# Performance work log

Hardware: AMD Instinct MI355X
Metric: run time of the kernel (lower is better)

Reference implementation:

```python
import jax, jax.numpy as jnp
import numpy as np

VOCAB=20000; EMB=300; FEAT=2052; HID=1024; OUT=3000; NK=8; NS=10; KOBJ=36; B=256; QLEN=14

def _wn(key, shape, scale=0.05):
    return jax.random.normal(key, shape, dtype=jnp.float32)*scale

def setup_inputs() -> dict:
    key = jax.random.key(0)
    ks = jax.random.split(key, 40)
    inp = {}
    inp['question'] = jax.random.randint(ks[0], (B, QLEN), 0, VOCAB)
    inp['image'] = jax.random.uniform(ks[1], (B, KOBJ, FEAT), dtype=jnp.float32)
    inp['K'] = KOBJ
    inp['qlen'] = jax.random.randint(ks[2], (B,), 1, QLEN+1)
    # params
    inp['wembed'] = _wn(ks[3], (VOCAB, EMB), 0.1)
    # GRU params (torch layout: W_ih [3H,E], W_hh [3H,H], biases [3H]) order r,z,n
    inp['gru_wih'] = _wn(ks[4], (3*HID, EMB))
    inp['gru_whh'] = _wn(ks[5], (3*HID, HID))
    inp['gru_bih'] = jnp.zeros((3*HID,), jnp.float32)
    inp['gru_bhh'] = jnp.zeros((3*HID,), jnp.float32)
    # img_attention (VisualAttention on feat_dim -> hid)
    inp['ia_img_w'] = _wn(ks[6], (HID, FEAT)); inp['ia_img_b'] = jnp.zeros((HID,), jnp.float32)
    inp['ia_txt_w'] = _wn(ks[7], (HID, HID)); inp['ia_txt_b'] = jnp.zeros((HID,), jnp.float32)
    inp['ia_att_w'] = _wn(ks[8], (1, HID)); inp['ia_att_b'] = jnp.zeros((1,), jnp.float32)
    # graph_attention (on feat_dim+hid -> hid)
    inp['ga_img_w'] = _wn(ks[9], (HID, FEAT+HID)); inp['ga_img_b'] = jnp.zeros((HID,), jnp.float32)
    inp['ga_txt_w'] = _wn(ks[10], (HID, HID)); inp['ga_txt_b'] = jnp.zeros((HID,), jnp.float32)
    inp['ga_att_w'] = _wn(ks[11], (1, HID)); inp['ga_att_b'] = jnp.zeros((1,), jnp.float32)
    # graph conv 1: feat_dim -> 2*hid, NK kernels, coord_dim=2
    inp['gc1_mu'] = _wn(ks[12], (NK, 2), 0.5)
    inp['gc1_sigma'] = jnp.ones((NK, 2), jnp.float32)*0.5
    inp['gc1_w'] = _wn(ks[13], (NK, FEAT, (2*HID)//NK), 0.02)
    inp['gc1_b'] = jnp.zeros((2*HID,), jnp.float32)
    # graph conv 2: 2*hid -> hid
    inp['gc2_mu'] = _wn(ks[14], (NK, 2), 0.5)
    inp['gc2_sigma'] = jnp.ones((NK, 2), jnp.float32)*0.5
    inp['gc2_w'] = _wn(ks[15], (NK, 2*HID, HID//NK), 0.02)
    inp['gc2_b'] = jnp.zeros((HID,), jnp.float32)
    # output heads
    inp['out1_w'] = _wn(ks[16], (OUT, HID)); inp['out1_b'] = jnp.zeros((OUT,), jnp.float32)
    inp['out2_w'] = _wn(ks[17], (OUT, OUT)); inp['out2_b'] = jnp.zeros((OUT,), jnp.float32)
    inp['iout1_w'] = _wn(ks[18], (OUT, HID)); inp['iout1_b'] = jnp.zeros((OUT,), jnp.float32)
    inp['iout2_w'] = _wn(ks[19], (OUT, OUT)); inp['iout2_b'] = jnp.zeros((OUT,), jnp.float32)
    return inp

def _gru_encode(question, qlen, wembed, wih, whh, bih, bhh):
    emb = wembed[question]  # [B,T,E]
    T = emb.shape[1]
    def step(h, xt_t):
        xt, t = xt_t
        gi = xt @ wih.T + bih
        gh = h @ whh.T + bhh
        ir, iz, inn = jnp.split(gi, 3, axis=-1)
        hr, hz, hn = jnp.split(gh, 3, axis=-1)
        r = jax.nn.sigmoid(ir + hr)
        z = jax.nn.sigmoid(iz + hz)
        n = jnp.tanh(inn + r*hn)
        hnew = (1-z)*n + z*h
        valid = (t < qlen)[:, None]
        h = jnp.where(valid, hnew, h)
        return h, None
    h0 = jnp.zeros((emb.shape[0], HID), emb.dtype)
    hT, _ = jax.lax.scan(step, h0, (jnp.swapaxes(emb,0,1), jnp.arange(T)))
    return hT

def _vis_att(img, q, img_w, img_b, txt_w, txt_b, att_w, att_b):
    img_proj = jax.nn.relu(img @ img_w.T + img_b)        # [B,L,H]
    q_proj = jax.nn.relu(q @ txt_w.T + txt_b)            # [B,H]
    joint = img_proj * q_proj[:, None, :]
    raw = joint @ att_w.T + att_b                         # [B,L,1]
    att = jax.nn.softmax(raw, axis=1)[..., 0]             # [B,L]
    img_att = jnp.einsum('bli,bl->bi', img, att)
    comb = jax.nn.relu(img_att @ img_w.T + img_b) * q_proj
    return att, comb

def _gauss_weights(pseudo, mu, sigma):
    # pseudo [B,N,N,2], mu/sigma [NK,2] -> [B,N,N,NK]
    diff = pseudo[..., None, :] - mu  # [B,N,N,NK,2]
    w = jnp.exp(-0.5 * jnp.sum((diff / (1e-14 + sigma))**2, axis=-1))
    return w

def _graph_conv(neigh, pseudo, mu, sigma, w, b):
    # neigh [B,N,N,Fin], pseudo [B,N,N,2], w [NK,Fin,Fout//NK]
    kw = _gauss_weights(pseudo, mu, sigma)                # [B,N,N,K]
    agg = jnp.einsum('bnmf,bnmk->bnkf', neigh, kw)        # weighted sum over neighbours
    out = jnp.einsum('bnkf,kfo->bnko', agg, w)            # per-kernel linear
    B_, N_, K_, O_ = out.shape
    return out.reshape(B_, N_, K_*O_) + b

def _compute_pseudo(bb_centre):
    d = bb_centre[:, :, None, :] - bb_centre[:, None, :, :]  # [B,N,N,2]
    rho = jnp.sqrt(d[..., 0]**2 + d[..., 1]**2)
    theta = jnp.arctan2(d[..., 0], d[..., 1])
    return jnp.stack((rho, theta), axis=-1)

def reference(question, image, K, qlen, wembed, gru_wih, gru_whh, gru_bih, gru_bhh,
              ia_img_w, ia_img_b, ia_txt_w, ia_txt_b, ia_att_w, ia_att_b,
              ga_img_w, ga_img_b, ga_txt_w, ga_txt_b, ga_att_w, ga_att_b,
              gc1_mu, gc1_sigma, gc1_w, gc1_b, gc2_mu, gc2_sigma, gc2_w, gc2_b,
              out1_w, out1_b, out2_w, out2_b, iout1_w, iout1_b, iout2_w, iout2_b):
    qenc = _gru_encode(question, qlen, wembed, gru_wih, gru_whh, gru_bih, gru_bhh)  # [B,H]
    att, img_ques_comb = _vis_att(image, qenc, ia_img_w, ia_img_b, ia_txt_w, ia_txt_b, ia_att_w, ia_att_b)
    _, topk_idx = jax.lax.top_k(att, NS)                  # [B,NS]
    topk_img = jnp.take_along_axis(image, topk_idx[:, :, None], axis=1)  # [B,NS,F]
    bb = topk_img[:, :, -4:]
    bb_size = bb[:, :, 2:] - bb[:, :, :2]
    bb_centre = bb[:, :, :2] + 0.5*bb_size
    pseudo = _compute_pseudo(bb_centre)                    # [B,NS,NS,2]
    neigh1 = jnp.broadcast_to(topk_img[:, None, :, :], (topk_img.shape[0], NS, NS, topk_img.shape[-1]))
    h1 = jax.nn.relu(_graph_conv(neigh1, pseudo, gc1_mu, gc1_sigma, gc1_w, gc1_b))  # [B,NS,2H]
    neigh2 = jnp.broadcast_to(h1[:, None, :, :], (h1.shape[0], NS, NS, h1.shape[-1]))
    h2 = jax.nn.relu(_graph_conv(neigh2, pseudo, gc2_mu, gc2_sigma, gc2_w, gc2_b))  # [B,NS,H]
    graph_nodes = jnp.concatenate((topk_img, h2), axis=2)  # [B,NS,F+H]
    g_att, graph_ques_comb = _vis_att(graph_nodes, qenc, ga_img_w, ga_img_b, ga_txt_w, ga_txt_b, ga_att_w, ga_att_b)
    logits_1 = jax.nn.relu(graph_ques_comb @ out1_w.T + out1_b) @ out2_w.T + out2_b
    logits_2 = jax.nn.relu(img_ques_comb @ iout1_w.T + iout1_b) @ iout2_w.T + iout2_b
    return logits_1 + logits_2
```

## Files before the change

kernel.cpp:

```cpp
#include <hip/hip_runtime.h>
#include <cmath>

#define VOCAB 20000
#define EMB 300
#define FEAT 2052
#define HID 1024
#define OUTN 3000
#define NK 8
#define NS 10
#define KOBJ 36
#define BATCH 256
#define QLEN_ 14

typedef __attribute__((ext_vector_type(8))) short bf8v;
typedef __attribute__((ext_vector_type(4))) float f4v;

__device__ __forceinline__ short f2bf(float f) {
    union { float f; unsigned u; } v; v.f = f;
    unsigned r = v.u + 0x7fff + ((v.u >> 16) & 1);
    return (short)(r >> 16);
}
__device__ __forceinline__ float bf2f(short h) {
    union { unsigned u; float f; } v; v.u = ((unsigned)(unsigned short)h) << 16;
    return v.f;
}

__device__ __forceinline__ void gload16(const short* g, short* l) {
    typedef __attribute__((address_space(1))) void gv;
    typedef __attribute__((address_space(3))) void lv;
    __builtin_amdgcn_global_load_lds((gv*)g, (lv*)l, 16, 0, 0);
}

template<int N> __device__ __forceinline__ void vmw() {
    asm volatile("s_waitcnt vmcnt(%0)" :: "n"(N) : "memory");
}
template<int PW> __device__ __forceinline__ void vmwait(int nf) {
    switch (nf) {
        case 0:  vmw<0>();      break;
        case 1:  vmw<1 * PW>(); break;
        case 2:  vmw<2 * PW>(); break;
        default: vmw<3 * PW>(); break;
    }
}

template<int PREC, int MI, int D>
__global__ __launch_bounds__(512)
void mgemm_k(const short* __restrict__ Ah_g, const short* __restrict__ Al_g, int lda,
             const short* __restrict__ Bh_g, const short* __restrict__ Bl_g, int ldb,
             float* __restrict__ Cf, int ldc,
             short* __restrict__ Cb, int ldcb,
             const float* __restrict__ bias,
             const float* __restrict__ mul, int ldmul,
             int Nvalid, int K, int beta, int relu)
{
    constexpr int BM  = MI * 32;
    constexpr int MIW = MI / 2;
    constexpr int ASZ = BM * 32;
    constexpr int BSZ = 128 * 32;
    constexpr int NBUF = (PREC == 3) ? 2 * D : D;
    __shared__ short SA[NBUF * ASZ];
    __shared__ short SB[NBUF * BSZ];

    int gx = gridDim.x;
    int flat = blockIdx.y * gx + blockIdx.x;
    int total = gx * gridDim.y;
    int bx, by;
    if ((total & 7) == 0) {
        int r = (flat & 7) * (total >> 3) + (flat >> 3);
        by = r / gx; bx = r - by * gx;
    } else { bx = blockIdx.x; by = blockIdx.y; }

    int tid = threadIdx.x;
    int lane = tid & 63, wid = tid >> 6;
    int m0 = by * BM, n0 = bx * 128;
    const short* Ab  = Ah_g + (size_t)m0 * lda;
    const short* Bb  = Bh_g + (size_t)n0 * ldb;
    const short* Abl = (PREC == 3) ? Al_g + (size_t)m0 * lda : nullptr;
    const short* Bbl = (PREC == 3) ? Bl_g + (size_t)n0 * ldb : nullptr;

    constexpr int AISS = BM / 16;
    constexpr int NISS = (PREC == 3) ? 2 * (AISS + 8) : (AISS + 8);
    constexpr int REM  = NISS & 7;
    constexpr int PWH  = (NISS + 7) >> 3;
    constexpr int PWL  = NISS >> 3;
    int rr = lane & 15;
    int cc = (lane >> 4) * 8;

    auto stage = [&](int q, int k0) {
        short* sa  = SA + q * ASZ;
        short* sb  = SB + q * BSZ;
        short* sal = SA + (D + q) * ASZ;
        short* sbl = SB + (D + q) * BSZ;
        #pragma unroll
        for (int t = wid; t < NISS; t += 8) {
            int u = t;
            const short* g; short* l;
            if (u < AISS)              {                   g = Ab  + (size_t)(u*16+rr)*lda + k0 + cc; l = sa  + u*512; }
            else if (u < AISS + 8)     { u -= AISS;        g = Bb  + (size_t)(u*16+rr)*ldb + k0 + cc; l = sb  + u*512; }
            else if (u < 2*AISS + 8)   { u -= AISS + 8;    g = Abl + (size_t)(u*16+rr)*lda + k0 + cc; l = sal + u*512; }
            else                       { u -= 2*AISS + 8;  g = Bbl + (size_t)(u*16+rr)*ldb + k0 + cc; l = sbl + u*512; }
            gload16(g, l);
        }
    };

    f4v acc[MIW][4] = {};
    int nk = K >> 5;
    int P = (D - 1 < nk) ? (D - 1) : nk;
    for (int q = 0; q < P; ++q) stage(q, q << 5);

    for (int kt = 0; kt < nk; ++kt) {
        int nxt = kt + D - 1;
        if (nxt < nk) stage(nxt & (D - 1), nxt << 5);
        int rem = nk - 1 - kt;
        int nf = rem < D - 1 ? rem : D - 1;
        if (REM == 0 || wid < REM) vmwait<PWH>(nf); else vmwait<PWL>(nf);
        __builtin_amdgcn_s_barrier();
        __builtin_amdgcn_sched_barrier(0);
        {
            int q = kt & (D - 1);
            int wy = wid >> 1, wx = wid & 1;
            int quad = lane >> 4, l15 = lane & 15;
            const bf8v* A8 = (const bf8v*)(SA + q * ASZ);
            const bf8v* B8 = (const bf8v*)(SB + q * BSZ);
            bf8v ah[MIW], bh[4];
            #pragma unroll
            for (int i = 0; i < MIW; i++) ah[i] = A8[(wy*MIW + i)*64 + quad*16 + l15];
            #pragma unroll
            for (int j = 0; j < 4; j++)   bh[j] = B8[(wx*4 + j)*64 + quad*16 + l15];
            if (PREC == 3) {
                const bf8v* A8l = (const bf8v*)(SA + (D + q) * ASZ);
                const bf8v* B8l = (const bf8v*)(SB + (D + q) * BSZ);
                bf8v al[MIW], bl[4];
                #pragma unroll
                for (int i = 0; i < MIW; i++) al[i] = A8l[(wy*MIW + i)*64 + quad*16 + l15];
                #pragma unroll
                for (int j = 0; j < 4; j++)   bl[j] = B8l[(wx*4 + j)*64 + quad*16 + l15];
                #pragma unroll
                for (int i = 0; i < MIW; i++)
                    #pragma unroll
                    for (int j = 0; j < 4; j++) {
                        acc[i][j] = __builtin_amdgcn_mfma_f32_16x16x32_bf16(ah[i], bh[j], acc[i][j], 0, 0, 0);
                        acc[i][j] = __builtin_amdgcn_mfma_f32_16x16x32_bf16(al[i], bh[j], acc[i][j], 0, 0, 0);
                        acc[i][j] = __builtin_amdgcn_mfma_f32_16x16x32_bf16(ah[i], bl[j], acc[i][j], 0, 0, 0);
                    }
            } else {
                #pragma unroll
                for (int i = 0; i < MIW; i++)
                    #pragma unroll
                    for (int j = 0; j < 4; j++)
                        acc[i][j] = __builtin_amdgcn_mfma_f32_16x16x32_bf16(ah[i], bh[j], acc[i][j], 0, 0, 0);
            }
        }
        __builtin_amdgcn_sched_barrier(0);
        __builtin_amdgcn_s_barrier();
        __builtin_amdgcn_sched_barrier(0);
    }

    int wy = wid >> 1, wx = wid & 1;
    int quad = lane >> 4, l15 = lane & 15;
    #pragma unroll
    for (int i = 0; i < MIW; i++) {
        int mb = m0 + wy * (MIW * 16) + i * 16 + quad * 4;
        #pragma unroll
        for (int j = 0; j < 4; j++) {
            int n = n0 + wx * 64 + j * 16 + l15;
            bool nin = n < Nvalid;
            #pragma unroll
            for (int r = 0; r < 4; r++) {
                int m = mb + r;
                float v = acc[i][j][r];
                if (nin) {
                    if (beta) v += Cf[(size_t)m * ldc + n];
                    if (bias) v += bias[n];
                    if (relu) v = fmaxf(v, 0.f);
                    if (mul)  v *= mul[(size_t)m * ldmul + n];
                    if (Cf) Cf[(size_t)m * ldc + n] = v;
                    if (Cb) Cb[(size_t)m * ldcb + n] = f2bf(v);
                } else if (Cb && n < ldcb) {
                    Cb[(size_t)m * ldcb + n] = 0;
                }
            }
        }
    }
}

static void mg(hipStream_t s, int prec, int mi,
               const short* Ah, const short* Al, int lda,
               const short* Bh, const short* Bl, int ldb,
               float* Cf, int ldc, short* Cb, int ldcb,
               const float* bias, const float* mul, int ldmul,
               int M, int N, int K, int beta, int relu)
{
    dim3 grid((N + 127) / 128, M / (mi * 32));
    if (prec == 3) {
        if (mi == 4) mgemm_k<3,4,2><<<grid,512,0,s>>>(Ah,Al,lda,Bh,Bl,ldb,Cf,ldc,Cb,ldcb,bias,mul,ldmul,N,K,beta,relu);
        else         mgemm_k<3,2,2><<<grid,512,0,s>>>(Ah,Al,lda,Bh,Bl,ldb,Cf,ldc,Cb,ldcb,bias,mul,ldmul,N,K,beta,relu);
    } else {
        if (mi == 4) mgemm_k<1,4,4><<<grid,512,0,s>>>(Ah,Al,lda,Bh,Bl,ldb,Cf,ldc,Cb,ldcb,bias,mul,ldmul,N,K,beta,relu);
        else         mgemm_k<1,2,4><<<grid,512,0,s>>>(Ah,Al,lda,Bh,Bl,ldb,Cf,ldc,Cb,ldcb,bias,mul,ldmul,N,K,beta,relu);
    }
}

__global__ void fill0_k(float* p, int n) {
    int i = blockIdx.x * 256 + threadIdx.x;
    if (i < n) p[i] = 0.f;
}

__global__ void cvt_k(const float* __restrict__ src, int sld, int srows, int scols,
                      short* __restrict__ hi, short* __restrict__ lo, int dld, int n) {
    int i = blockIdx.x * 256 + threadIdx.x;
    if (i >= n) return;
    int r = i / dld, c = i - r * dld;
    float v = (r < srows && c < scols) ? src[(size_t)r * sld + c] : 0.f;
    short h = f2bf(v);
    hi[i] = h;
    if (lo) lo[i] = f2bf(v - bf2f(h));
}

__global__ void embed_k(const int* __restrict__ q, const float* __restrict__ wemb,
                        short* __restrict__ hi, short* __restrict__ lo) {
    int i = blockIdx.x * 256 + threadIdx.x;
    if (i >= BATCH * QLEN_ * 320) return;
    int c = i % 320; int bt = i / 320;
    float v = (c < EMB) ? wemb[(size_t)q[bt] * EMB + c] : 0.f;
    short h = f2bf(v);
    hi[i] = h;
    lo[i] = f2bf(v - bf2f(h));
}

__global__ void gru_point_k(const float* __restrict__ gi, int ldgi, const float* __restrict__ gh,
                            const int* __restrict__ qlen, float* __restrict__ h,
                            short* __restrict__ qh, short* __restrict__ ql, int t) {
    int i = blockIdx.x * 256 + threadIdx.x;
    if (i >= BATCH * HID) return;
    int b = i / HID; int j = i % HID;
    float ir = gi[(size_t)b * ldgi + j];
    float iz = gi[(size_t)b * ldgi + HID + j];
    float in = gi[(size_t)b * ldgi + 2 * HID + j];
    float hr = gh[(size_t)b * 3 * HID + j];
    float hz = gh[(size_t)b * 3 * HID + HID + j];
    float hn = gh[(size_t)b * 3 * HID + 2 * HID + j];
    float r = 1.f / (1.f + expf(-(ir + hr)));
    float z = 1.f / (1.f + expf(-(iz + hz)));
    float n = tanhf(in + r * hn);
    float hold = h[i];
    float val = (t < qlen[b]) ? ((1.f - z) * n + z * hold) : hold;
    h[i] = val;
    short hh = f2bf(val);
    qh[i] = hh;
    ql[i] = f2bf(val - bf2f(hh));
}

__global__ __launch_bounds__(256)
void attraw_k(const float* __restrict__ proj, const float* __restrict__ qproj,
              const float* __restrict__ attw, const float* __restrict__ attb,
              float* __restrict__ raw, int L) {
    int wave = blockIdx.x * 4 + (threadIdx.x >> 6);
    int lane = threadIdx.x & 63;
    if (wave >= BATCH * L) return;
    int b = wave / L;
    const float* p = proj + (size_t)wave * HID;
    const float* q = qproj + (size_t)b * HID;
    float s = 0.f;
    for (int hh = lane; hh < HID; hh += 64) s += p[hh] * q[hh] * attw[hh];
    #pragma unroll
    for (int o = 32; o; o >>= 1) s += __shfl_down(s, o, 64);
    if (lane == 0) raw[wave] = s + attb[0];
}

__global__ void softmax_k(float* raw, int L) {
    int b = blockIdx.x * blockDim.x + threadIdx.x;
    if (b >= BATCH) return;
    float* r = raw + (size_t)b * L;
    float mx = -1e30f;
    for (int l = 0; l < L; l++) mx = fmaxf(mx, r[l]);
    float sum = 0.f;
    for (int l = 0; l < L; l++) { float e = expf(r[l] - mx); r[l] = e; sum += e; }
    float inv = 1.f / sum;
    for (int l = 0; l < L; l++) r[l] *= inv;
}

__global__ void wsumb_k(const float* __restrict__ src, int sF, const float* __restrict__ att,
                        int L, short* __restrict__ outh, int dld, int n) {
    int i = blockIdx.x * 256 + threadIdx.x;
    if (i >= n) return;
    int c = i % dld; int b = i / dld;
    float s = 0.f;
    if (c < sF)
        for (int l = 0; l < L; l++) s += src[((size_t)b * L + l) * sF + c] * att[b * L + l];
    outh[i] = f2bf(s);
}

__global__ void topk_k(const float* __restrict__ att, int* __restrict__ idx) {
    int b = blockIdx.x * blockDim.x + threadIdx.x;
    if (b >= BATCH) return;
    float v[KOBJ]; bool taken[KOBJ];
    for (int l = 0; l < KOBJ; l++) { v[l] = att[(size_t)b * KOBJ + l]; taken[l] = false; }
    for (int s = 0; s < NS; s++) {
        float best = -1e30f; int bi = 0;
        for (int l = 0; l < KOBJ; l++)
            if (!taken[l] && v[l] > best) { best = v[l]; bi = l; }
        taken[bi] = true;
        idx[b * NS + s] = bi;
    }
}

__global__ void gather_k(const float* __restrict__ img, const int* __restrict__ idx,
                         float* __restrict__ outf, short* __restrict__ outh) {
    int i = blockIdx.x * 256 + threadIdx.x;
    if (i >= BATCH * NS * 2080) return;
    int c = i % 2080; int bs = i / 2080; int b = bs / NS; int s = bs % NS;
    float v = 0.f;
    if (c < FEAT) {
        v = img[((size_t)b * KOBJ + idx[b * NS + s]) * FEAT + c];
        outf[(size_t)bs * FEAT + c] = v;
    }
    outh[i] = f2bf(v);
}

__global__ void kw_k(const float* __restrict__ image, const int* __restrict__ tidx,
                     const float* __restrict__ mu1, const float* __restrict__ sig1,
                     const float* __restrict__ mu2, const float* __restrict__ sig2,
                     float* __restrict__ kw1, float* __restrict__ kw2) {
    int i = blockIdx.x * blockDim.x + threadIdx.x;
    if (i >= BATCH * NS * NS) return;
    int m = i % NS; int bn = i / NS; int b = bn / NS; int n = bn % NS;
    const float* bbn = image + ((size_t)b * KOBJ + tidx[b * NS + n]) * FEAT + (FEAT - 4);
    const float* bbm = image + ((size_t)b * KOBJ + tidx[b * NS + m]) * FEAT + (FEAT - 4);
    float cnx = bbn[0] + 0.5f * (bbn[2] - bbn[0]);
    float cny = bbn[1] + 0.5f * (bbn[3] - bbn[1]);
    float cmx = bbm[0] + 0.5f * (bbm[2] - bbm[0]);
    float cmy = bbm[1] + 0.5f * (bbm[3] - bbm[1]);
    float d0 = cnx - cmx, d1 = cny - cmy;
    float rho = sqrtf(d0 * d0 + d1 * d1);
    float theta = atan2f(d0, d1);
    #pragma unroll
    for (int k = 0; k < NK; k++) {
        float a1 = (rho   - mu1[k * 2 + 0]) / (1e-14f + sig1[k * 2 + 0]);
        float b1 = (theta - mu1[k * 2 + 1]) / (1e-14f + sig1[k * 2 + 1]);
        kw1[(size_t)i * NK + k] = expf(-0.5f * (a1 * a1 + b1 * b1));
        float a2 = (rho   - mu2[k * 2 + 0]) / (1e-14f + sig2[k * 2 + 0]);
        float b2 = (theta - mu2[k * 2 + 1]) / (1e-14f + sig2[k * 2 + 1]);
        kw2[(size_t)i * NK + k] = expf(-0.5f * (a2 * a2 + b2 * b2));
    }
}

__global__ void mix_k(const float* __restrict__ Y, const float* __restrict__ kw,
                      const float* __restrict__ bias, short* __restrict__ outh,
                      float* __restrict__ outf, int KO, int CT) {
    int i = blockIdx.x * blockDim.x + threadIdx.x;
    if (i >= BATCH * NS * CT) return;
    int c = i % CT; int bn = i / CT; int b = bn / NS;
    int k = c / KO;
    float s = bias[c];
    const float* kwp = kw + ((size_t)bn * NS) * NK + k;
    const float* Yp  = Y + ((size_t)b * NS) * CT + c;
    #pragma unroll
    for (int m = 0; m < NS; m++) s += kwp[m * NK] * Yp[(size_t)m * CT];
    s = fmaxf(s, 0.f);
    outh[i] = f2bf(s);
    if (outf) outf[i] = s;
}

__global__ void packcvt_k(const float* __restrict__ src, short* __restrict__ dst,
                          int S, int O, int dld) {
    __shared__ float t[32][33];
    int k = blockIdx.z;
    const float* s = src + (size_t)k * S * O;
    short* d = dst + (size_t)k * O * dld;
    int f0 = blockIdx.y * 32, o0 = blockIdx.x * 32;
    for (int i = threadIdx.y; i < 32; i += 8) {
        int f = f0 + i, o = o0 + threadIdx.x;
        t[i][threadIdx.x] = (f < S && o < O) ? s[(size_t)f * O + o] : 0.f;
    }
    __syncthreads();
    for (int i = threadIdx.y; i < 32; i += 8) {
        int o = o0 + i, f = f0 + threadIdx.x;
        if (o < O && f < dld) d[(size_t)o * dld + f] = f2bf(t[threadIdx.x][i]);
    }
}

extern "C" void kernel_launch(void* const* d_in, const int* in_sizes, int n_in,
                              void* d_out, int out_size, void* d_ws, size_t ws_size,
                              hipStream_t stream)
{
    const int*   question  = (const int*)d_in[0];
    const float* image     = (const float*)d_in[1];
    const int*   qlen      = (const int*)d_in[3];
    const float* wembed    = (const float*)d_in[4];
    const float* gru_wih   = (const float*)d_in[5];
    const float* gru_whh   = (const float*)d_in[6];
    const float* gru_bih   = (const float*)d_in[7];
    const float* gru_bhh   = (const float*)d_in[8];
    const float* ia_img_w  = (const float*)d_in[9];
    const float* ia_img_b  = (const float*)d_in[10];
    const float* ia_txt_w  = (const float*)d_in[11];
    const float* ia_txt_b  = (const float*)d_in[12];
    const float* ia_att_w  = (const float*)d_in[13];
    const float* ia_att_b  = (const float*)d_in[14];
    const float* ga_img_w  = (const float*)d_in[15];
    const float* ga_img_b  = (const float*)d_in[16];
    const float* ga_txt_w  = (const float*)d_in[17];
    const float* ga_txt_b  = (const float*)d_in[18];
    const float* ga_att_w  = (const float*)d_in[19];
    const float* ga_att_b  = (const float*)d_in[20];
    const float* gc1_mu    = (const float*)d_in[21];
    const float* gc1_sigma = (const float*)d_in[22];
    const float* gc1_w     = (const float*)d_in[23];
    const float* gc1_b     = (const float*)d_in[24];
    const float* gc2_mu    = (const float*)d_in[25];
    const float* gc2_sigma = (const float*)d_in[26];
    const float* gc2_w     = (const float*)d_in[27];
    const float* gc2_b     = (const float*)d_in[28];
    const float* out1_w    = (const float*)d_in[29];
    const float* out1_b    = (const float*)d_in[30];
    const float* out2_w    = (const float*)d_in[31];
    const float* out2_b    = (const float*)d_in[32];
    const float* iout1_w   = (const float*)d_in[33];
    const float* iout1_b   = (const float*)d_in[34];
    const float* iout2_w   = (const float*)d_in[35];
    const float* iout2_b   = (const float*)d_in[36];
    float* out = (float*)d_out;

    float* ws = (float*)d_ws;
    size_t off = 0;
    auto alloc  = [&](size_t n)   { size_t o = off; off += (n + 63) & ~(size_t)63; return ws + o; };
    auto allocS = [&](size_t nsh) { return (short*)alloc((nsh + 1) >> 1); };

    float* qenc   = alloc((size_t)BATCH * HID);
    float* att_ia = alloc((size_t)BATCH * KOBJ);
    float* att_ga = alloc((size_t)BATCH * NS);
    int*   tidx   = (int*)alloc((size_t)BATCH * NS);
    float* timg_f = alloc((size_t)2560 * FEAT);
    float* kw1    = alloc((size_t)BATCH * NS * NS * NK);
    float* kw2    = alloc((size_t)BATCH * NS * NS * NK);
    short* wih_h   = allocS((size_t)3072 * 320);  short* wih_l   = allocS((size_t)3072 * 320);
    short* whh_h   = allocS((size_t)3072 * 1024); short* whh_l   = allocS((size_t)3072 * 1024);
    short* iaimg_h = allocS((size_t)1024 * 2080); short* iaimg_l = allocS((size_t)1024 * 2080);
    short* iatxt_h = allocS((size_t)1024 * 1024); short* iatxt_l = allocS((size_t)1024 * 1024);
    short* emb_h   = allocS((size_t)3584 * 320);  short* emb_l   = allocS((size_t)3584 * 320);
    short* qenc_h  = allocS((size_t)256 * 1024);  short* qenc_l  = allocS((size_t)256 * 1024);
    float* R1 = alloc(12500000);
    float* U  = alloc(19200000);

    float* gi_all = R1;
    float* gh     = R1 + 11010048;
    float* improj = R1;
    float* qproj  = R1 + 9437184;
    short* img_h  = (short*)U;
    short* img_l  = (short*)U + 19169280;
    short* imatt_h = (short*)U + 13189120;
    float* Y1 = R1;
    float* Y2 = R1 + 5242880;
    short* gc1t_h = (short*)(R1 + 7864320);
    short* gc2t_h = (short*)(R1 + 7864320) + 4259840;
    short* timg_h = (short*)U;
    short* h1_h   = (short*)U + 5324800;
    short* h2_h   = (short*)U + 10567680;
    float* h2_f   = (float*)((short*)U + 20807680);
    float* gproj   = R1;
    float* qproj2  = R1 + 2621440;
    float* gtmp    = R1 + 2883584;
    short* gatt_img_h = (short*)U + 13721600;
    short* gatt_h2_h  = (short*)U + 14254080;
    short* gcomb_h = (short*)U + 14516224;
    short* icomb_h = (short*)U + 14778368;
    short* hid1_h  = (short*)U + 15040512;
    short* hid2_h  = (short*)U + 15810560;
    short* gaw_img_h = (short*)U + 16580608;
    short* gaw_h2_h  = (short*)U + 18710528;
    short* gatxt_h   = (short*)U + 19759104;
    short* o1w_h  = (short*)R1;
    short* io1w_h = (short*)R1 + 3145728;
    short* o2w_h  = (short*)R1 + 6291456;
    short* io2w_h = (short*)R1 + 15532032;

    auto NB = [](size_t n) { return (unsigned)((n + 255) / 256); };

    cvt_k<<<NB(983040),  256, 0, stream>>>(gru_wih, 300, 3072, 300, wih_h, wih_l, 320, 983040);
    cvt_k<<<NB(3145728), 256, 0, stream>>>(gru_whh, 1024, 3072, 1024, whh_h, whh_l, 1024, 3145728);
    cvt_k<<<NB(2129920), 256, 0, stream>>>(ia_img_w, FEAT, 1024, FEAT, iaimg_h, iaimg_l, 2080, 2129920);
    cvt_k<<<NB(1048576), 256, 0, stream>>>(ia_txt_w, 1024, 1024, 1024, iatxt_h, iatxt_l, 1024, 1048576);
    cvt_k<<<NB(19169280),256, 0, stream>>>(image, FEAT, 9216, FEAT, img_h, img_l, 2080, 19169280);
    embed_k<<<NB(1146880), 256, 0, stream>>>(question, wembed, emb_h, emb_l);
    fill0_k<<<NB(262144), 256, 0, stream>>>(qenc, 262144);
    fill0_k<<<NB(262144), 256, 0, stream>>>((float*)qenc_h, 262144);

    mg(stream, 3, 4, emb_h, emb_l, 320, wih_h, wih_l, 320, gi_all, 3072, nullptr, 0,
       gru_bih, nullptr, 0, 3584, 3072, 320, 0, 0);
    for (int t = 0; t < QLEN_; t++) {
        mg(stream, 3, 2, qenc_h, qenc_l, 1024, whh_h, whh_l, 1024, gh, 3072, nullptr, 0,
           gru_bhh, nullptr, 0, 256, 3072, 1024, 0, 0);
        gru_point_k<<<NB(262144), 256, 0, stream>>>(gi_all + (size_t)t * 3 * HID, QLEN_ * 3 * HID,
                                                    gh, qlen, qenc, qenc_h, qenc_l, t);
    }

    mg(stream, 3, 4, img_h, img_l, 2080, iaimg_h, iaimg_l, 2080, improj, 1024, nullptr, 0,
       ia_img_b, nullptr, 0, 9216, 1024, 2080, 0, 1);
    mg(stream, 3, 2, qenc_h, qenc_l, 1024, iatxt_h, iatxt_l, 1024, qproj, 1024, nullptr, 0,
       ia_txt_b, nullptr, 0, 256, 1024, 1024, 0, 1);
    attraw_k<<<(BATCH * KOBJ) / 4, 256, 0, stream>>>(improj, qproj, ia_att_w, ia_att_b, att_ia, KOBJ);
    softmax_k<<<1, 256, 0, stream>>>(att_ia, KOBJ);
    wsumb_k<<<NB(532480), 256, 0, stream>>>(image, FEAT, att_ia, KOBJ, imatt_h, 2080, 532480);
    mg(stream, 1, 2, imatt_h, nullptr, 2080, iaimg_h, nullptr, 2080, nullptr, 0, icomb_h, 1024,
       ia_img_b, qproj, 1024, 256, 1024, 2080, 0, 1);

    topk_k<<<1, 256, 0, stream>>>(att_ia, tidx);
    gather_k<<<NB(5324800), 256, 0, stream>>>(image, tidx, timg_f, timg_h);
    kw_k<<<NB(25600), 256, 0, stream>>>(image, tidx, gc1_mu, gc1_sigma, gc2_mu, gc2_sigma, kw1, kw2);
    packcvt_k<<<dim3(8, 65, NK), dim3(32, 8), 0, stream>>>(gc1_w, gc1t_h, FEAT, 256, 2080);
    packcvt_k<<<dim3(4, 64, NK), dim3(32, 8), 0, stream>>>(gc2_w, gc2t_h, 2048, 128, 2048);
    mg(stream, 1, 4, timg_h, nullptr, 2080, gc1t_h, nullptr, 2080, Y1, 2048, nullptr, 0,
       nullptr, nullptr, 0, 2560, 2048, 2080, 0, 0);
    mix_k<<<NB(5242880), 256, 0, stream>>>(Y1, kw1, gc1_b, h1_h, nullptr, 256, 2048);
    mg(stream, 1, 4, h1_h, nullptr, 2048, gc2t_h, nullptr, 2048, Y2, 1024, nullptr, 0,
       nullptr, nullptr, 0, 2560, 1024, 2048, 0, 0);
    mix_k<<<NB(2621440), 256, 0, stream>>>(Y2, kw2, gc2_b, h2_h, h2_f, 128, 1024);

    cvt_k<<<NB(2129920), 256, 0, stream>>>(ga_img_w, FEAT + HID, 1024, FEAT, gaw_img_h, nullptr, 2080, 2129920);
    cvt_k<<<NB(1048576), 256, 0, stream>>>(ga_img_w + FEAT, FEAT + HID, 1024, HID, gaw_h2_h, nullptr, 1024, 1048576);
    cvt_k<<<NB(1048576), 256, 0, stream>>>(ga_txt_w, 1024, 1024, 1024, gatxt_h, nullptr, 1024, 1048576);
    mg(stream, 1, 4, timg_h, nullptr, 2080, gaw_img_h, nullptr, 2080, gproj, 1024, nullptr, 0,
       nullptr, nullptr, 0, 2560, 1024, 2080, 0, 0);
    mg(stream, 1, 4, h2_h, nullptr, 1024, gaw_h2_h, nullptr, 1024, gproj, 1024, nullptr, 0,
       ga_img_b, nullptr, 0, 2560, 1024, 1024, 1, 1);
    mg(stream, 1, 2, qenc_h, nullptr, 1024, gatxt_h, nullptr, 1024, qproj2, 1024, nullptr, 0,
       ga_txt_b, nullptr, 0, 256, 1024, 1024, 0, 1);
    attraw_k<<<(BATCH * NS) / 4, 256, 0, stream>>>(gproj, qproj2, ga_att_w, ga_att_b, att_ga, NS);
    softmax_k<<<1, 256, 0, stream>>>(att_ga, NS);
    wsumb_k<<<NB(532480), 256, 0, stream>>>(timg_f, FEAT, att_ga, NS, gatt_img_h, 2080, 532480);
    wsumb_k<<<NB(262144), 256, 0, stream>>>(h2_f, HID, att_ga, NS, gatt_h2_h, 1024, 262144);
    mg(stream, 1, 2, gatt_img_h, nullptr, 2080, gaw_img_h, nullptr, 2080, gtmp, 1024, nullptr, 0,
       nullptr, nullptr, 0, 256, 1024, 2080, 0, 0);
    mg(stream, 1, 2, gatt_h2_h, nullptr, 1024, gaw_h2_h, nullptr, 1024, gtmp, 1024, gcomb_h, 1024,
       ga_img_b, qproj2, 1024, 256, 1024, 1024, 1, 1);

    cvt_k<<<NB(3145728), 256, 0, stream>>>(out1_w, 1024, OUTN, 1024, o1w_h, nullptr, 1024, 3145728);
    cvt_k<<<NB(3145728), 256, 0, stream>>>(iout1_w, 1024, OUTN, 1024, io1w_h, nullptr, 1024, 3145728);
    cvt_k<<<NB(9240576), 256, 0, stream>>>(out2_w, OUTN, OUTN, OUTN, o2w_h, nullptr, 3008, 9240576);
    cvt_k<<<NB(9240576), 256, 0, stream>>>(iout2_w, OUTN, OUTN, OUTN, io2w_h, nullptr, 3008, 9240576);
    mg(stream, 1, 2, gcomb_h, nullptr, 1024, o1w_h, nullptr, 1024, nullptr, 0, hid1_h, 3008,
       out1_b, nullptr, 0, 256, OUTN, 1024, 0, 1);
    mg(stream, 1, 2, icomb_h, nullptr, 1024, io1w_h, nullptr, 1024, nullptr, 0, hid2_h, 3008,
       iout1_b, nullptr, 0, 256, OUTN, 1024, 0, 1);
    mg(stream, 1, 2, hid1_h, nullptr, 3008, o2w_h, nullptr, 3008, out, OUTN, nullptr, 0,
       out2_b, nullptr, 0, 256, OUTN, 3008, 0, 0);
    mg(stream, 1, 2, hid2_h, nullptr, 3008, io2w_h, nullptr, 3008, out, OUTN, nullptr, 0,
       iout2_b, nullptr, 0, 256, OUTN, 3008, 1, 0);
}
```

Baseline: 1.768 ms.

## Batch paired GEMMs into one launch, split-K GRU recurrence, rewrite graph mix kernel

Extends the GEMM kernel so one launch can run two independent problems by duplicating the grid in y. This is used to split the GRU hidden-state GEMM into two K halves that are summed in the pointwise kernel, and to run the two output-head GEMM chains side by side, adding their results at the end. It also adds an XCD-aware block remap, switches the large GEMMs to 256-row tiles (MI=8), and rewrites the graph-conv mix kernel to stage kernel weights in shared memory and reuse each Y load across all NS outputs. The aim is to fill more CUs on small GEMMs, cut launch count, and reduce redundant global reads. The cost is extra temporary buffers, an extra add kernel, and MI=8 tiles that may raise register and LDS pressure.

```diff
diff --git a/kernel.cpp b/kernel.cpp
--- a/kernel.cpp
+++ b/kernel.cpp
@@ -47,11 +47,15 @@
 __global__ __launch_bounds__(512)
 void mgemm_k(const short* __restrict__ Ah_g, const short* __restrict__ Al_g, int lda,
              const short* __restrict__ Bh_g, const short* __restrict__ Bl_g, int ldb,
-             float* __restrict__ Cf, int ldc,
-             short* __restrict__ Cb, int ldcb,
-             const float* __restrict__ bias,
-             const float* __restrict__ mul, int ldmul,
-             int Nvalid, int K, int beta, int relu)
+             float* __restrict__ Cf_g, int ldc,
+             short* __restrict__ Cb_g, int ldcb,
+             const float* __restrict__ bias_g,
+             const float* __restrict__ mul_g, int ldmul,
+             int Nvalid, int K, int beta, int relu,
+             const short* __restrict__ A2h, const short* __restrict__ A2l,
+             const short* __restrict__ B2h, const short* __restrict__ B2l,
+             float* __restrict__ C2f, short* __restrict__ C2b,
+             const float* __restrict__ bias2)
 {
     constexpr int BM  = MI * 32;
     constexpr int MIW = MI / 2;
@@ -61,22 +65,41 @@
     __shared__ short SA[NBUF * ASZ];
     __shared__ short SB[NBUF * BSZ];
 
-    int gx = gridDim.x;
+    int gx = gridDim.x, gy = gridDim.y;
     int flat = blockIdx.y * gx + blockIdx.x;
-    int total = gx * gridDim.y;
+    int total = gx * gy;
     int bx, by;
-    if ((total & 7) == 0) {
+    if ((total & 7) == 0 && (gx & 7) == 0) {
+        int xcd = flat & 7, r = flat >> 3;
+        int cpx = gx >> 3;
+        int col = r / gy;
+        bx = xcd * cpx + col;
+        by = r - col * gy;
+    } else if ((total & 7) == 0) {
         int r = (flat & 7) * (total >> 3) + (flat >> 3);
         by = r / gx; bx = r - by * gx;
     } else { bx = blockIdx.x; by = blockIdx.y; }
 
+    const short *pAh = Ah_g, *pAl = Al_g, *pBh = Bh_g, *pBl = Bl_g;
+    float* pCf = Cf_g; short* pCb = Cb_g;
+    const float* pbias = bias_g; const float* pmul = mul_g;
+    int pbeta = beta;
+    if (A2h) {
+        int yh = gy >> 1;
+        if (by >= yh) {
+            by -= yh;
+            pAh = A2h; pAl = A2l; pBh = B2h; pBl = B2l;
+            pCf = C2f; pCb = C2b; pbias = bias2; pmul = nullptr; pbeta = 0;
+        }
+    }
+
     int tid = threadIdx.x;
     int lane = tid & 63, wid = tid >> 6;
     int m0 = by * BM, n0 = bx * 128;
-    const short* Ab  = Ah_g + (size_t)m0 * lda;
-    const short* Bb  = Bh_g + (size_t)n0 * ldb;
-    const short* Abl = (PREC == 3) ? Al_g + (size_t)m0 * lda : nullptr;
-    const short* Bbl = (PREC == 3) ? Bl_g + (size_t)n0 * ldb : nullptr;
+    const short* Ab  = pAh + (size_t)m0 * lda;
+    const short* Bb  = pBh + (size_t)n0 * ldb;
+    const short* Abl = (PREC == 3) ? pAl + (size_t)m0 * lda : nullptr;
+    const short* Bbl = (PREC == 3) ? pBl + (size_t)n0 * ldb : nullptr;
 
     constexpr int AISS = BM / 16;
     constexpr int NISS = (PREC == 3) ? 2 * (AISS + 8) : (AISS + 8);
@@ -110,14 +133,14 @@
 
     for (int kt = 0; kt < nk; ++kt) {
         int nxt = kt + D - 1;
-        if (nxt < nk) stage(nxt & (D - 1), nxt << 5);
+        if (nxt < nk) stage(nxt % D, nxt << 5);
         int rem = nk - 1 - kt;
         int nf = rem < D - 1 ? rem : D - 1;
         if (REM == 0 || wid < REM) vmwait<PWH>(nf); else vmwait<PWL>(nf);
         __builtin_amdgcn_s_barrier();
         __builtin_amdgcn_sched_barrier(0);
         {
-            int q = kt & (D - 1);
+            int q = kt % D;
             int wy = wid >> 1, wx = wid & 1;
             int quad = lane >> 4, l15 = lane & 15;
             const bf8v* A8 = (const bf8v*)(SA + q * ASZ);
@@ -170,18 +193,43 @@
                 int m = mb + r;
                 float v = acc[i][j][r];
                 if (nin) {
-                    if (beta) v += Cf[(size_t)m * ldc + n];
-                    if (bias) v += bias[n];
-                    if (relu) v = fmaxf(v, 0.f);
-                    if (mul)  v *= mul[(size_t)m * ldmul + n];
-                    if (Cf) Cf[(size_t)m * ldc + n] = v;
-                    if (Cb) Cb[(size_t)m * ldcb + n] = f2bf(v);
-                } else if (Cb && n < ldcb) {
-                    Cb[(size_t)m * ldcb + n] = 0;
+                    if (pbeta) v += pCf[(size_t)m * ldc + n];
+                    if (pbias) v += pbias[n];
+                    if (relu)  v = fmaxf(v, 0.f);
+                    if (pmul)  v *= pmul[(size_t)m * ldmul + n];
+                    if (pCf) pCf[(size_t)m * ldc + n] = v;
+                    if (pCb) pCb[(size_t)m * ldcb + n] = f2bf(v);
+                } else if (pCb && n < ldcb) {
+                    pCb[(size_t)m * ldcb + n] = 0;
                 }
             }
         }
     }
+}
+
+static void mgx(hipStream_t s, int prec, int mi,
+                const short* Ah, const short* Al, int lda,
+                const short* Bh, const short* Bl, int ldb,
+                float* Cf, int ldc, short* Cb, int ldcb,
+                const float* bias, const float* mul, int ldmul,
+                int M, int N, int K, int beta, int relu,
+                int ydup,
+                const short* A2h, const short* A2l,
+                const short* B2h, const short* B2l,
+                float* C2f, short* C2b, const float* bias2)
+{
+    dim3 grid((N + 127) / 128, (M / (mi * 32)) * ydup);
+    #define ARGS Ah,Al,lda,Bh,Bl,ldb,Cf,ldc,Cb,ldcb,bias,mul,ldmul,N,K,beta,relu,A2h,A2l,B2h,B2l,C2f,C2b,bias2
+    if (prec == 3) {
+        if      (mi == 8) mgemm_k<3,8,2><<<grid,512,0,s>>>(ARGS);
+        else if (mi == 4) mgemm_k<3,4,2><<<grid,512,0,s>>>(ARGS);
+        else              mgemm_k<3,2,2><<<grid,512,0,s>>>(ARGS);
+    } else {
+        if      (mi == 8) mgemm_k<1,8,4><<<grid,512,0,s>>>(ARGS);
+        else if (mi == 4) mgemm_k<1,4,4><<<grid,512,0,s>>>(ARGS);
+        else              mgemm_k<1,2,4><<<grid,512,0,s>>>(ARGS);
+    }
+    #undef ARGS
 }
 
 static void mg(hipStream_t s, int prec, int mi,
@@ -191,14 +239,8 @@
                const float* bias, const float* mul, int ldmul,
                int M, int N, int K, int beta, int relu)
 {
-    dim3 grid((N + 127) / 128, M / (mi * 32));
-    if (prec == 3) {
-        if (mi == 4) mgemm_k<3,4,2><<<grid,512,0,s>>>(Ah,Al,lda,Bh,Bl,ldb,Cf,ldc,Cb,ldcb,bias,mul,ldmul,N,K,beta,relu);
-        else         mgemm_k<3,2,2><<<grid,512,0,s>>>(Ah,Al,lda,Bh,Bl,ldb,Cf,ldc,Cb,ldcb,bias,mul,ldmul,N,K,beta,relu);
-    } else {
-        if (mi == 4) mgemm_k<1,4,4><<<grid,512,0,s>>>(Ah,Al,lda,Bh,Bl,ldb,Cf,ldc,Cb,ldcb,bias,mul,ldmul,N,K,beta,relu);
-        else         mgemm_k<1,2,4><<<grid,512,0,s>>>(Ah,Al,lda,Bh,Bl,ldb,Cf,ldc,Cb,ldcb,bias,mul,ldmul,N,K,beta,relu);
-    }
+    mgx(s, prec, mi, Ah, Al, lda, Bh, Bl, ldb, Cf, ldc, Cb, ldcb, bias, mul, ldmul,
+        M, N, K, beta, relu, 1, nullptr, nullptr, nullptr, nullptr, nullptr, nullptr, nullptr);
 }
 
 __global__ void fill0_k(float* p, int n) {
@@ -229,6 +271,7 @@
 }
 
 __global__ void gru_point_k(const float* __restrict__ gi, int ldgi, const float* __restrict__ gh,
+                            const float* __restrict__ gh2,
                             const int* __restrict__ qlen, float* __restrict__ h,
                             short* __restrict__ qh, short* __restrict__ ql, int t) {
     int i = blockIdx.x * 256 + threadIdx.x;
@@ -237,9 +280,9 @@
     float ir = gi[(size_t)b * ldgi + j];
     float iz = gi[(size_t)b * ldgi + HID + j];
     float in = gi[(size_t)b * ldgi + 2 * HID + j];
-    float hr = gh[(size_t)b * 3 * HID + j];
-    float hz = gh[(size_t)b * 3 * HID + HID + j];
-    float hn = gh[(size_t)b * 3 * HID + 2 * HID + j];
+    float hr = gh[(size_t)b * 3 * HID + j]          + gh2[(size_t)b * 3 * HID + j];
+    float hz = gh[(size_t)b * 3 * HID + HID + j]    + gh2[(size_t)b * 3 * HID + HID + j];
+    float hn = gh[(size_t)b * 3 * HID + 2 * HID + j]+ gh2[(size_t)b * 3 * HID + 2 * HID + j];
     float r = 1.f / (1.f + expf(-(ir + hr)));
     float z = 1.f / (1.f + expf(-(iz + hz)));
     float n = tanhf(in + r * hn);
@@ -345,21 +388,41 @@
     }
 }
 
-__global__ void mix_k(const float* __restrict__ Y, const float* __restrict__ kw,
-                      const float* __restrict__ bias, short* __restrict__ outh,
-                      float* __restrict__ outf, int KO, int CT) {
-    int i = blockIdx.x * blockDim.x + threadIdx.x;
-    if (i >= BATCH * NS * CT) return;
-    int c = i % CT; int bn = i / CT; int b = bn / NS;
+__global__ __launch_bounds__(256)
+void mixn_k(const float* __restrict__ Y, const float* __restrict__ kw,
+            const float* __restrict__ bias, short* __restrict__ outh,
+            float* __restrict__ outf, int KO, int CT) {
+    __shared__ float kws[NS * NS * NK];
+    int b = blockIdx.y;
+    for (int i = threadIdx.x; i < NS * NS * NK; i += 256)
+        kws[i] = kw[(size_t)b * (NS * NS * NK) + i];
+    __syncthreads();
+    int c = blockIdx.x * 256 + threadIdx.x;
     int k = c / KO;
-    float s = bias[c];
-    const float* kwp = kw + ((size_t)bn * NS) * NK + k;
-    const float* Yp  = Y + ((size_t)b * NS) * CT + c;
+    const float* Yp = Y + ((size_t)b * NS) * CT + c;
+    float acc[NS];
     #pragma unroll
-    for (int m = 0; m < NS; m++) s += kwp[m * NK] * Yp[(size_t)m * CT];
-    s = fmaxf(s, 0.f);
-    outh[i] = f2bf(s);
-    if (outf) outf[i] = s;
+    for (int n = 0; n < NS; n++) acc[n] = 0.f;
+    #pragma unroll
+    for (int m = 0; m < NS; m++) {
+        float y = Yp[(size_t)m * CT];
+        #pragma unroll
+        for (int n = 0; n < NS; n++) acc[n] += kws[n * (NS * NK) + m * NK + k] * y;
+    }
+    float bc = bias[c];
+    #pragma unroll
+    for (int n = 0; n < NS; n++) {
+        float s = fmaxf(acc[n] + bc, 0.f);
+        size_t o = ((size_t)b * NS + n) * CT + c;
+        outh[o] = f2bf(s);
+        if (outf) outf[o] = s;
+    }
+}
+
+__global__ void addout_k(const float* __restrict__ t1, const float* __restrict__ t2,
+                         float* __restrict__ out, int n) {
+    int i = blockIdx.x * 256 + threadIdx.x;
+    if (i < n) out[i] = t1[i] + t2[i];
 }
 
 __global__ void packcvt_k(const float* __restrict__ src, short* __restrict__ dst,
@@ -440,11 +503,12 @@
     short* iatxt_h = allocS((size_t)1024 * 1024); short* iatxt_l = allocS((size_t)1024 * 1024);
     short* emb_h   = allocS((size_t)3584 * 320);  short* emb_l   = allocS((size_t)3584 * 320);
     short* qenc_h  = allocS((size_t)256 * 1024);  short* qenc_l  = allocS((size_t)256 * 1024);
-    float* R1 = alloc(12500000);
+    float* R1 = alloc(12600000);
     float* U  = alloc(19200000);
 
     float* gi_all = R1;
     float* gh     = R1 + 11010048;
+    float* gh2    = R1 + 11796480;
     float* improj = R1;
     float* qproj  = R1 + 9437184;
     short* img_h  = (short*)U;
@@ -470,6 +534,8 @@
     short* gaw_img_h = (short*)U + 16580608;
     short* gaw_h2_h  = (short*)U + 18710528;
     short* gatxt_h   = (short*)U + 19759104;
+    float* tmp1 = (float*)((short*)U + 26050560);
+    float* tmp2 = tmp1 + 768000;
     short* o1w_h  = (short*)R1;
     short* io1w_h = (short*)R1 + 3145728;
     short* o2w_h  = (short*)R1 + 6291456;
@@ -486,16 +552,17 @@
     fill0_k<<<NB(262144), 256, 0, stream>>>(qenc, 262144);
     fill0_k<<<NB(262144), 256, 0, stream>>>((float*)qenc_h, 262144);
 
-    mg(stream, 3, 4, emb_h, emb_l, 320, wih_h, wih_l, 320, gi_all, 3072, nullptr, 0,
+    mg(stream, 3, 8, emb_h, emb_l, 320, wih_h, wih_l, 320, gi_all, 3072, nullptr, 0,
        gru_bih, nullptr, 0, 3584, 3072, 320, 0, 0);
     for (int t = 0; t < QLEN_; t++) {
-        mg(stream, 3, 2, qenc_h, qenc_l, 1024, whh_h, whh_l, 1024, gh, 3072, nullptr, 0,
-           gru_bhh, nullptr, 0, 256, 3072, 1024, 0, 0);
+        mgx(stream, 3, 2, qenc_h, qenc_l, 1024, whh_h, whh_l, 1024, gh, 3072, nullptr, 0,
+            gru_bhh, nullptr, 0, 256, 3072, 512, 0, 0,
+            2, qenc_h + 512, qenc_l + 512, whh_h + 512, whh_l + 512, gh2, nullptr, nullptr);
         gru_point_k<<<NB(262144), 256, 0, stream>>>(gi_all + (size_t)t * 3 * HID, QLEN_ * 3 * HID,
-                                                    gh, qlen, qenc, qenc_h, qenc_l, t);
-    }
-
-    mg(stream, 3, 4, img_h, img_l, 2080, iaimg_h, iaimg_l, 2080, improj, 1024, nullptr, 0,
+                                                    gh, gh2, qlen, qenc, qenc_h, qenc_l, t);
+    }
+
+    mg(stream, 3, 8, img_h, img_l, 2080, iaimg_h, iaimg_l, 2080, improj, 1024, nullptr, 0,
        ia_img_b, nullptr, 0, 9216, 1024, 2080, 0, 1);
     mg(stream, 3, 2, qenc_h, qenc_l, 1024, iatxt_h, iatxt_l, 1024, qproj, 1024, nullptr, 0,
        ia_txt_b, nullptr, 0, 256, 1024, 1024, 0, 1);
@@ -512,10 +579,10 @@
     packcvt_k<<<dim3(4, 64, NK), dim3(32, 8), 0, stream>>>(gc2_w, gc2t_h, 2048, 128, 2048);
     mg(stream, 1, 4, timg_h, nullptr, 2080, gc1t_h, nullptr, 2080, Y1, 2048, nullptr, 0,
        nullptr, nullptr, 0, 2560, 2048, 2080, 0, 0);
-    mix_k<<<NB(5242880), 256, 0, stream>>>(Y1, kw1, gc1_b, h1_h, nullptr, 256, 2048);
+    mixn_k<<<dim3(8, BATCH), 256, 0, stream>>>(Y1, kw1, gc1_b, h1_h, nullptr, 256, 2048);
     mg(stream, 1, 4, h1_h, nullptr, 2048, gc2t_h, nullptr, 2048, Y2, 1024, nullptr, 0,
        nullptr, nullptr, 0, 2560, 1024, 2048, 0, 0);
-    mix_k<<<NB(2621440), 256, 0, stream>>>(Y2, kw2, gc2_b, h2_h, h2_f, 128, 1024);
+    mixn_k<<<dim3(4, BATCH), 256, 0, stream>>>(Y2, kw2, gc2_b, h2_h, h2_f, 128, 1024);
 
     cvt_k<<<NB(2129920), 256, 0, stream>>>(ga_img_w, FEAT + HID, 1024, FEAT, gaw_img_h, nullptr, 2080, 2129920);
     cvt_k<<<NB(1048576), 256, 0, stream>>>(ga_img_w + FEAT, FEAT + HID, 1024, HID, gaw_h2_h, nullptr, 1024, 1048576);
@@ -539,12 +606,11 @@
     cvt_k<<<NB(3145728), 256, 0, stream>>>(iout1_w, 1024, OUTN, 1024, io1w_h, nullptr, 1024, 3145728);
     cvt_k<<<NB(9240576), 256, 0, stream>>>(out2_w, OUTN, OUTN, OUTN, o2w_h, nullptr, 3008, 9240576);
     cvt_k<<<NB(9240576), 256, 0, stream>>>(iout2_w, OUTN, OUTN, OUTN, io2w_h, nullptr, 3008, 9240576);
-    mg(stream, 1, 2, gcomb_h, nullptr, 1024, o1w_h, nullptr, 1024, nullptr, 0, hid1_h, 3008,
-       out1_b, nullptr, 0, 256, OUTN, 1024, 0, 1);
-    mg(stream, 1, 2, icomb_h, nullptr, 1024, io1w_h, nullptr, 1024, nullptr, 0, hid2_h, 3008,
-       iout1_b, nullptr, 0, 256, OUTN, 1024, 0, 1);
-    mg(stream, 1, 2, hid1_h, nullptr, 3008, o2w_h, nullptr, 3008, out, OUTN, nullptr, 0,
-       out2_b, nullptr, 0, 256, OUTN, 3008, 0, 0);
-    mg(stream, 1, 2, hid2_h, nullptr, 3008, io2w_h, nullptr, 3008, out, OUTN, nullptr, 0,
-       iout2_b, nullptr, 0, 256, OUTN, 3008, 1, 0);
-}
+    mgx(stream, 1, 2, gcomb_h, nullptr, 1024, o1w_h, nullptr, 1024, nullptr, 0, hid1_h, 3008,
+        out1_b, nullptr, 0, 256, OUTN, 1024, 0, 1,
+        2, icomb_h, nullptr, io1w_h, nullptr, nullptr, hid2_h, iout1_b);
+    mgx(stream, 1, 2, hid1_h, nullptr, 3008, o2w_h, nullptr, 3008, tmp1, 3000, nullptr, 0,
+        out2_b, nullptr, 0, 256, OUTN, 3008, 0, 0,
+        2, hid2_h, nullptr, io2w_h, nullptr, tmp2, nullptr, iout2_b);
+    addout_k<<<NB(768000), 256, 0, stream>>>(tmp1, tmp2, out, 768000);
+}
```

Result: faster. 1.666 ms (-5.7%).
